# Performance work log

Measured on AMD Instinct MI355X. Metric: run time of the kernel, lower is better.

The kernel has to match this reference:

```python
import jax, jax.numpy as jnp
import numpy as np

B, C, H, W = 4, 64, 128, 128
DG = 16            # deformable groups
K = 9              # 3x3 kernel taps
MAX_RES = 10.0     # max_residue_magnitude


def conv3x3(x, w, b):
    y = jax.lax.conv_general_dilated(x, w, (1, 1), 'SAME',
                                     dimension_numbers=('NCHW', 'OIHW', 'NCHW'))
    return y + b[None, :, None, None]


def lrelu(x):
    return jnp.where(x >= 0, x, 0.1 * x)


def deform_conv(x, offset, mask, w, b):
    # x: [B,C,H,W]; offset: [B,2*DG*K,H,W] (dy,dx interleaved per tap); mask: [B,DG*K,H,W]
    Bx, Cx, Hx, Wx = x.shape
    Cg = Cx // DG
    off = offset.reshape(Bx, DG, K, 2, Hx, Wx)
    dy, dx = off[:, :, :, 0], off[:, :, :, 1]          # [B,DG,K,H,W]
    ky = (jnp.arange(K) // 3 - 1).astype(x.dtype)      # kernel tap row offsets (pad=1, dil=1)
    kx = (jnp.arange(K) % 3 - 1).astype(x.dtype)
    hh = jnp.arange(Hx, dtype=x.dtype)
    ww = jnp.arange(Wx, dtype=x.dtype)
    py = dy + ky[None, None, :, None, None] + hh[None, None, None, :, None]
    px = dx + kx[None, None, :, None, None] + ww[None, None, None, None, :]
    y0 = jnp.floor(py)
    x0 = jnp.floor(px)
    ly = py - y0
    lx = px - x0
    y0i = y0.astype(jnp.int32)
    x0i = x0.astype(jnp.int32)
    flat = x.reshape(Bx, DG, Cg, Hx * Wx)

    def gather(yi, xi):
        valid = (yi >= 0) & (yi < Hx) & (xi >= 0) & (xi < Wx)
        idx = jnp.clip(yi, 0, Hx - 1) * Wx + jnp.clip(xi, 0, Wx - 1)
        g = jnp.take_along_axis(flat, idx.reshape(Bx, DG, 1, K * Hx * Wx), axis=3)
        g = g.reshape(Bx, DG, Cg, K, Hx, Wx)
        return g * valid[:, :, None].astype(g.dtype)

    samp = (gather(y0i, x0i) * ((1 - ly) * (1 - lx))[:, :, None]
            + gather(y0i, x0i + 1) * ((1 - ly) * lx)[:, :, None]
            + gather(y0i + 1, x0i) * (ly * (1 - lx))[:, :, None]
            + gather(y0i + 1, x0i + 1) * (ly * lx)[:, :, None])   # [B,DG,Cg,K,H,W]
    samp = samp * mask.reshape(Bx, DG, 1, K, Hx, Wx)
    samp = samp.reshape(Bx, Cx, K, Hx, Wx)
    wk = w.reshape(w.shape[0], Cx, K)
    return jnp.einsum('bckhw,ock->bohw', samp, wk) + b[None, :, None, None]


def setup_inputs() -> dict:
    key = jax.random.key(0)
    ks = jax.random.split(key, 12)
    in_off = 2 * C + 2  # (1 + pa_frames//2)*C + pa_frames, pa_frames=2

    def n(k, shape, s=0.05):
        return jax.random.normal(k, shape, jnp.float32) * s

    return {
        'x': n(ks[0], (B, C, H, W), 1.0),
        'x_flow_warped': n(ks[1], (B, C, H, W), 1.0),
        'x_current': n(ks[2], (B, C, H, W), 1.0),
        'flow': n(ks[3], (B, 2, H, W), 1.0),
        'w0': n(ks[4], (C, in_off, 3, 3)), 'b0': jnp.zeros((C,), jnp.float32),
        'w1': n(ks[5], (C, C, 3, 3)), 'b1': jnp.zeros((C,), jnp.float32),
        'w2': n(ks[6], (C, C, 3, 3)), 'b2': jnp.zeros((C,), jnp.float32),
        'w3': n(ks[7], (3 * K * DG, C, 3, 3)), 'b3': jnp.zeros((3 * K * DG,), jnp.float32),
        'w_dcn': n(ks[8], (C, C, 3, 3)), 'b_dcn': jnp.zeros((C,), jnp.float32),
    }


def reference(x, x_flow_warped, x_current, flow,
              w0, b0, w1, b1, w2, b2, w3, b3, w_dcn, b_dcn):
    # conv_offset stack on [warped feats, current feats, flow]
    concat = jnp.concatenate([x_flow_warped, x_current, flow], axis=1)
    h = lrelu(conv3x3(concat, w0, b0))
    h = lrelu(conv3x3(h, w1, b1))
    h = lrelu(conv3x3(h, w2, b2))
    out = conv3x3(h, w3, b3)
    o1, o2, m = jnp.split(out, 3, axis=1)
    offset = MAX_RES * jnp.tanh(jnp.concatenate([o1, o2], axis=1))   # [B,2*DG*K,H,W]
    # pa_frames == 2: add flipped flow (dy,dx) to every tap's offset pair
    offset = offset + jnp.tile(flow[:, ::-1], (1, offset.shape[1] // 2, 1, 1))
    mask = jax.nn.sigmoid(m)
    return deform_conv(x, offset, mask, w_dcn, b_dcn)
```

## Files before the change

kernel.cpp:

```cpp
#include <hip/hip_runtime.h>
#include <hip/hip_bf16.h>
#include <cmath>

#define HH 128
#define WW 128
#define HWSZ (HH*WW)
#define BB 4
#define PH 130

typedef __attribute__((ext_vector_type(8))) short short8;
typedef __attribute__((ext_vector_type(4))) short sh4;
typedef _Float16 half8 __attribute__((ext_vector_type(8)));
typedef __attribute__((ext_vector_type(16))) float f32x16;

__device__ __forceinline__ ushort f16_rn(float f) {
    _Float16 h = (_Float16)f;
    return __builtin_bit_cast(ushort, h);
}
__device__ __forceinline__ float f16_f(ushort u) {
    return (float)__builtin_bit_cast(_Float16, u);
}
__device__ __forceinline__ float fast_tanh(float x) {
    const float e = __builtin_amdgcn_exp2f(x * 2.885390081777927f);
    return 1.f - 2.f * __builtin_amdgcn_rcpf(e + 1.f);
}
__device__ __forceinline__ float fast_sig(float x) {
    return __builtin_amdgcn_rcpf(1.f + __builtin_amdgcn_exp2f(-x * 1.4426950408889634f));
}

__global__ __launch_bounds__(256) void prep_wcm(const float* __restrict__ w,
                                                ushort* __restrict__ wOut,
                                                int ICREAL, int ICPAD) {
    const int ICSTEPS = ICPAD >> 4;
    int idx = blockIdx.x * 256 + threadIdx.x;
    if (idx >= 9 * ICSTEPS * 64 * 16) return;
    int j = idx & 7, lhi = (idx >> 3) & 1, oc = (idx >> 4) & 63, tk = idx >> 10;
    int tap = tk / ICSTEPS, ks = tk - tap * ICSTEPS;
    int ic = ks * 16 + lhi * 8 + j;
    float v = (ic < ICREAL) ? w[(size_t)oc * ICREAL * 9 + ic * 9 + tap] : 0.f;
    wOut[idx] = f16_rn(v);
}

__global__ __launch_bounds__(256) void prep_w3cm(const float* __restrict__ w,
                                                 ushort* __restrict__ wOut) {
    int idx = blockIdx.x * 256 + threadIdx.x;
    if (idx >= 36 * 512 * 16) return;
    int j = idx & 7, lhi = (idx >> 3) & 1, oc = (idx >> 4) & 511, tk = idx >> 13;
    int tap = tk >> 2, ks = tk & 3;
    int ic = ks * 16 + lhi * 8 + j;
    float v = (oc < 432) ? w[(size_t)oc * 576 + ic * 9 + tap] : 0.f;
    wOut[idx] = f16_rn(v);
}

__global__ __launch_bounds__(256) void prep_wdf_k(const float* __restrict__ w,
                                                  ushort* __restrict__ whiF) {
    int idx = blockIdx.x * 256 + threadIdx.x;
    if (idx >= 64 * 576) return;
    int oc = idx / 576, rem = idx - oc * 576;
    int k9 = rem / 64, c = rem & 63;
    float v = w[(size_t)oc * 576 + c * 9 + k9];
    const int hv = c >> 5, r = c & 31;
    const int ks = r >> 4, lhi = (r >> 3) & 1, j = r & 7;
    const size_t dst = (size_t)((k9 * 2 + hv) * 2 + ks) * 1024 + oc * 16 + lhi * 8 + j;
    whiF[dst] = f16_rn(v);
}

__global__ __launch_bounds__(256) void zero_border(ushort* __restrict__ buf, int C) {
    int idx = blockIdx.x * 256 + threadIdx.x;
    if (idx >= BB * 4 * PH * C) return;
    int c = idx % C;
    int r = idx / C;
    int pos = r % PH;
    int zone = (r / PH) & 3;
    int b = r / (PH * 4);
    int y, x;
    if (zone == 0)      { y = 0;      x = pos; }
    else if (zone == 1) { y = PH - 1; x = pos; }
    else if (zone == 2) { y = pos;    x = 0; }
    else                { y = pos;    x = PH - 1; }
    buf[(((size_t)b * PH + y) * PH + x) * C + c] = 0;
}

__global__ __launch_bounds__(256) void cvt_cm(const float* __restrict__ xfw,
                                              const float* __restrict__ xcur,
                                              const float* __restrict__ flow,
                                              ushort* __restrict__ out) {
    __shared__ ushort T[32][36];
    const int tid = threadIdx.x;
    const int b = blockIdx.x >> 7, y = blockIdx.x & 127;

    for (int c0 = 0; c0 < 144; c0 += 32) {
        for (int x0 = 0; x0 < 128; x0 += 32) {
            #pragma unroll
            for (int i = 0; i < 4; ++i) {
                const int cl = i * 8 + (tid >> 5);
                const int c = c0 + cl;
                const int x = x0 + (tid & 31);
                float v = 0.f;
                if (c < 64)       v = xfw [((size_t)b * 64 + c)       * HWSZ + y * WW + x];
                else if (c < 128) v = xcur[((size_t)b * 64 + c - 64)  * HWSZ + y * WW + x];
                else if (c < 130) v = flow[((size_t)b * 2  + c - 128) * HWSZ + y * WW + x];
                T[cl][tid & 31] = f16_rn(v);
            }
            __syncthreads();
            #pragma unroll
            for (int i = 0; i < 4; ++i) {
                const int xl = i * 8 + (tid >> 5);
                const int c = c0 + (tid & 31);
                if (c < 144)
                    out[(((size_t)b * PH + y + 1) * PH + x0 + xl + 1) * 144 + c] = T[tid & 31][xl];
            }
            __syncthreads();
        }
    }
}

__global__ __launch_bounds__(256) void pack_x_k(const float* __restrict__ x,
                                                sh4* __restrict__ xP) {
    int idx = blockIdx.x * 256 + threadIdx.x;
    if (idx >= BB * 16 * HWSZ) return;
    int b = idx / (16 * HWSZ);
    int rem = idx - b * 16 * HWSZ;
    int dg = rem / HWSZ, pix = rem - dg * HWSZ;
    const float* src = x + ((size_t)b * 64 + dg * 4) * HWSZ + pix;
    sh4 v;
    v[0] = (short)f16_rn(src[0]);
    v[1] = (short)f16_rn(src[HWSZ]);
    v[2] = (short)f16_rn(src[2 * HWSZ]);
    v[3] = (short)f16_rn(src[3 * HWSZ]);
    xP[idx] = v;
}

template<int ICPAD, int ICSTEPS>
__global__ __launch_bounds__(512, 4) void conv_cm(
    const ushort* __restrict__ actIn, const ushort* __restrict__ wT,
    const float* __restrict__ bias, ushort* __restrict__ actOut)
{
    constexpr int SYI = PH * ICPAD;
    const int tid = threadIdx.x;
    const int id  = blockIdx.x;
    const int orig = (id & 7) * 64 + (id >> 3);
    const int b = orig >> 7, y = orig & 127;

    const int wave = tid >> 6, lane = tid & 63;
    const int wm = wave >> 2, wn = wave & 3;
    const int l31 = lane & 31, lhi = lane >> 5;

    f32x16 acc = {};

    const ushort* arow = actIn + ((size_t)b * PH + y) * SYI
                       + (wn * 32 + l31) * ICPAD + lhi * 8;
    const ushort* wb = wT + (wm * 32 + l31) * 16 + lhi * 8;

    #pragma unroll
    for (int tap = 0; tap < 9; ++tap) {
        const int ky = tap / 3, kx = tap % 3;
        #pragma unroll
        for (int ks = 0; ks < ICSTEPS; ++ks) {
            const half8 af = __builtin_bit_cast(half8,
                *(const short8*)&arow[ky * SYI + kx * ICPAD + ks * 16]);
            const half8 wf = __builtin_bit_cast(half8,
                *(const short8*)&wb[(size_t)(tap * ICSTEPS + ks) * 1024]);
            acc = __builtin_amdgcn_mfma_f32_32x32x16_f16(af, wf, acc, 0, 0, 0);
        }
    }

    const int oc = wm * 32 + l31;
    const float bi = bias[oc];
    ushort* ob = actOut + (((size_t)b * PH + y + 1) * PH + 1) * 64 + oc;
    #pragma unroll
    for (int r = 0; r < 16; ++r) {
        const int px = wn * 32 + (r & 3) + 8 * (r >> 2) + 4 * lhi;
        float v = acc[r] + bi;
        v = v >= 0.f ? v : 0.1f * v;
        ob[(size_t)px * 64] = f16_rn(v);
    }
}

__global__ __launch_bounds__(512, 2) void conv_lds(
    const ushort* __restrict__ actIn, const ushort* __restrict__ wT,
    const float* __restrict__ bias, ushort* __restrict__ actOut)
{
    __shared__ ushort aS[3 * 130 * 64];

    const int tid = threadIdx.x;
    const int id  = blockIdx.x;
    const int orig = (id & 7) * 64 + (id >> 3);
    const int b = orig >> 7, y = orig & 127;

    const int wave = tid >> 6, lane = tid & 63;
    const int wm = wave >> 2, wn = wave & 3;
    const int l31 = lane & 31, lhi = lane >> 5;

    for (int i = tid; i < 3 * 130 * 8; i += 512) {
        const int seg = i & 7;
        const int px  = (i >> 3) % 130;
        const int row = (i >> 3) / 130;
        const ushort* src = actIn + (((size_t)b * PH + y + row) * PH + px) * 64 + seg * 8;
        const int d16 = (row * 130 + px) * 8 + (seg ^ (px & 7));
        *(short8*)&aS[d16 * 8] = *(const short8*)src;
    }
    __syncthreads();

    f32x16 acc = {};
    const ushort* wb = wT + (wm * 32 + l31) * 16 + lhi * 8;

    #pragma unroll
    for (int tap = 0; tap < 9; ++tap) {
        const int ky = tap / 3, kx = tap % 3;
        #pragma unroll
        for (int ks = 0; ks < 4; ++ks) {
            const int lpx = wn * 32 + l31 + kx;
            const int idx16 = (ky * 130 + lpx) * 8 + ((ks * 2 + lhi) ^ (lpx & 7));
            const half8 af = __builtin_bit_cast(half8,
                *(const short8*)&aS[idx16 * 8]);
            const half8 wf = __builtin_bit_cast(half8,
                *(const short8*)&wb[(size_t)(tap * 4 + ks) * 1024]);
            acc = __builtin_amdgcn_mfma_f32_32x32x16_f16(af, wf, acc, 0, 0, 0);
        }
    }

    const int oc = wm * 32 + l31;
    const float bi = bias[oc];
    ushort* ob = actOut + (((size_t)b * PH + y + 1) * PH + 1) * 64 + oc;
    #pragma unroll
    for (int r = 0; r < 16; ++r) {
        const int px = wn * 32 + (r & 3) + 8 * (r >> 2) + 4 * lhi;
        float v = acc[r] + bi;
        v = v >= 0.f ? v : 0.1f * v;
        ob[(size_t)px * 64] = f16_rn(v);
    }
}

__global__ __launch_bounds__(512, 4) void conv3_cm(
    const ushort* __restrict__ actIn, const ushort* __restrict__ wT3,
    const float* __restrict__ bias, uint* __restrict__ offP,
    ushort* __restrict__ mskP, const float* __restrict__ flow)
{
    __shared__ ushort aS[3 * 66 * 64];

    const int tid = threadIdx.x;
    const int id  = blockIdx.x;
    const int orig = (id & 7) * 128 + (id >> 3);
    const int xhalf = orig & 1;
    const int rid = orig >> 1;
    const int b = rid >> 7, y = rid & 127;
    const int xb = xhalf * 64;

    const int wave = tid >> 6, lane = tid & 63;
    const int l31 = lane & 31, lhi = lane >> 5;
    const int o0 = wave * 64;

    for (int i = tid; i < 3 * 66 * 8; i += 512) {
        const int seg = i & 7;
        const int px  = (i >> 3) % 66;
        const int row = (i >> 3) / 66;
        const ushort* src = actIn + (((size_t)b * PH + y + row) * PH + xb + px) * 64 + seg * 8;
        const int d16 = (row * 66 + px) * 8 + (seg ^ (px & 7));
        *(short8*)&aS[d16 * 8] = *(const short8*)src;
    }
    __syncthreads();

    f32x16 acc[2][2] = {};
    const ushort* wb = wT3 + (o0 + l31) * 16 + lhi * 8;

    #pragma unroll
    for (int tap = 0; tap < 9; ++tap) {
        const int ky = tap / 3, kx = tap % 3;
        #pragma unroll
        for (int ks = 0; ks < 4; ++ks) {
            const half8 af0 = __builtin_bit_cast(half8,
                *(const short8*)&wb[(size_t)(tap * 4 + ks) * 8192]);
            const half8 af1 = __builtin_bit_cast(half8,
                *(const short8*)&wb[(size_t)(tap * 4 + ks) * 8192 + 512]);
            #pragma unroll
            for (int pg = 0; pg < 2; ++pg) {
                const int lpx = pg * 32 + l31 + kx;
                const int idx16 = (ky * 66 + lpx) * 8 + ((ks * 2 + lhi) ^ (lpx & 7));
                const half8 bf = __builtin_bit_cast(half8,
                    *(const short8*)&aS[idx16 * 8]);
                acc[0][pg] = __builtin_amdgcn_mfma_f32_32x32x16_f16(af0, bf, acc[0][pg], 0, 0, 0);
                acc[1][pg] = __builtin_amdgcn_mfma_f32_32x32x16_f16(af1, bf, acc[1][pg], 0, 0, 0);
            }
        }
    }

    uint*   offb = offP + (size_t)b * 144 * HWSZ;
    ushort* mskb = mskP + (size_t)b * 144 * HWSZ;
    #pragma unroll
    for (int pg = 0; pg < 2; ++pg) {
        const int px = xb + pg * 32 + l31;
        const size_t pixb = (size_t)y * WW + px;
        const float fl0 = flow[((size_t)b * 2)     * HWSZ + pixb];
        const float fl1 = flow[((size_t)b * 2 + 1) * HWSZ + pixb];
        #pragma unroll
        for (int mg = 0; mg < 2; ++mg) {
            #pragma unroll
            for (int t = 0; t < 8; ++t) {
                const int r0 = 2 * t;
                const int oc = o0 + mg * 32 + (r0 & 3) + 8 * (r0 >> 2) + 4 * lhi;
                const float vy = acc[mg][pg][r0]     + bias[oc < 432 ? oc : 0];
                const float vx = acc[mg][pg][r0 + 1] + bias[oc < 431 ? oc + 1 : 0];
                if (oc < 288) {
                    const float ry = 10.f * fast_tanh(vy) + fl1;
                    const float rx = 10.f * fast_tanh(vx) + fl0;
                    offb[(size_t)(oc >> 1) * HWSZ + pixb] =
                        (uint)f16_rn(ry) | ((uint)f16_rn(rx) << 16);
                } else if (oc < 432) {
                    mskb[(size_t)(oc - 288) * HWSZ + pixb] = f16_rn(fast_sig(vy));
                    mskb[(size_t)(oc - 287) * HWSZ + pixb] = f16_rn(fast_sig(vx));
                }
            }
        }
    }
}

__global__ __launch_bounds__(512, 4) void deform_v11(
    const sh4* __restrict__ xP, const uint* __restrict__ offP,
    const ushort* __restrict__ mskP, const ushort* __restrict__ wdfh,
    const float* __restrict__ bias, float* __restrict__ outp)
{
    __shared__ float red[2][2][64][33];

    const int tid = threadIdx.x;
    const int id  = blockIdx.x;
    const int orig = (id & 7) * 128 + (id >> 3);
    const int x0 = (orig & 1) * 64;
    const int rl = orig >> 1;
    const int y = rl & 127, b = rl >> 7;

    const int wave = tid >> 6, lane = tid & 63;
    const int l31 = lane & 31, lhi = lane >> 5;
    const int pxh = wave >> 2;
    const int w4  = wave & 3;
    const int k9h = w4 >> 1;
    const int hv  = w4 & 1;

    const int xp  = x0 + pxh * 32 + l31;
    const int pix = y * WW + xp;
    const uint*   offb = offP + (size_t)b * 144 * HWSZ;
    const ushort* mskb = mskP + (size_t)b * 144 * HWSZ;
    const float fy = (float)y, fx = (float)xp;

    f32x16 acc[2] = {};

    const int k9lo = k9h ? 5 : 0;
    const int k9hi = k9h ? 9 : 5;
    for (int k9 = k9lo; k9 < k9hi; ++k9) {
        const float kyf = (float)(k9 / 3 - 1);
        const float kxf = (float)(k9 % 3 - 1);
        #pragma unroll
        for (int ks = 0; ks < 2; ++ks) {
            short8 bfs;
            #pragma unroll
            for (int d2 = 0; d2 < 2; ++d2) {
                const int dg = hv * 8 + ks * 4 + lhi * 2 + d2;
                const int m  = dg * 9 + k9;
                const uint u = offb[(size_t)m * HWSZ + pix];
                const float dy = f16_f((ushort)(u & 0xffffu));
                const float dx = f16_f((ushort)(u >> 16));
                const float mk = f16_f(mskb[(size_t)m * HWSZ + pix]);
                const float py = dy + kyf + fy;
                const float px = dx + kxf + fx;
                const float y0f = floorf(py), x0f = floorf(px);
                const float ly = py - y0f, lx = px - x0f;
                const int yi = (int)y0f, xi = (int)x0f;
                const float w00 = (1.f - ly) * (1.f - lx), w01 = (1.f - ly) * lx;
                const float w10 = ly * (1.f - lx),         w11 = ly * lx;
                const bool vy0 = (unsigned)yi < (unsigned)HH, vy1 = (unsigned)(yi + 1) < (unsigned)HH;
                const bool vx0 = (unsigned)xi < (unsigned)WW, vx1 = (unsigned)(xi + 1) < (unsigned)WW;
                const float f00 = (vy0 && vx0) ? w00 * mk : 0.f;
                const float f01 = (vy0 && vx1) ? w01 * mk : 0.f;
                const float f10 = (vy1 && vx0) ? w10 * mk : 0.f;
                const float f11 = (vy1 && vx1) ? w11 * mk : 0.f;
                const int cy0 = min(max(yi, 0), HH - 1), cy1 = min(max(yi + 1, 0), HH - 1);
                const int cx0 = min(max(xi, 0), WW - 1), cx1 = min(max(xi + 1, 0), WW - 1);
                const sh4* xg = xP + (size_t)(b * 16 + dg) * HWSZ;
                const sh4 c00 = xg[cy0 * WW + cx0], c01 = xg[cy0 * WW + cx1];
                const sh4 c10 = xg[cy1 * WW + cx0], c11 = xg[cy1 * WW + cx1];
                #pragma unroll
                for (int n = 0; n < 4; ++n) {
                    const float s = f00 * f16_f((ushort)c00[n]) + f01 * f16_f((ushort)c01[n])
                                  + f10 * f16_f((ushort)c10[n]) + f11 * f16_f((ushort)c11[n]);
                    bfs[d2 * 4 + n] = (short)f16_rn(s);
                }
            }
            const half8 bf = __builtin_bit_cast(half8, bfs);
            const size_t abase = (size_t)((k9 * 2 + hv) * 2 + ks) * 1024 + l31 * 16 + lhi * 8;
            #pragma unroll
            for (int mg = 0; mg < 2; ++mg) {
                const half8 ah = __builtin_bit_cast(half8, *(const short8*)&wdfh[abase + mg * 512]);
                acc[mg] = __builtin_amdgcn_mfma_f32_32x32x16_f16(ah, bf, acc[mg], 0, 0, 0);
            }
        }
    }

    if (w4 >= 2) {
        #pragma unroll
        for (int mg = 0; mg < 2; ++mg)
            #pragma unroll
            for (int r = 0; r < 16; ++r)
                red[pxh][w4 - 2][lane][mg * 16 + r] = acc[mg][r];
    }
    __syncthreads();
    if (w4 < 2) {
        #pragma unroll
        for (int mg = 0; mg < 2; ++mg)
            #pragma unroll
            for (int r = 0; r < 16; ++r)
                acc[mg][r] += red[pxh][w4][lane][mg * 16 + r];
    }
    __syncthreads();
    if (w4 == 1) {
        #pragma unroll
        for (int mg = 0; mg < 2; ++mg)
            #pragma unroll
            for (int r = 0; r < 16; ++r)
                red[pxh][0][lane][mg * 16 + r] = acc[mg][r];
    }
    __syncthreads();
    if (w4 == 0) {
        #pragma unroll
        for (int mg = 0; mg < 2; ++mg)
            #pragma unroll
            for (int r = 0; r < 16; ++r) {
                const int oc = mg * 32 + (r & 3) + 8 * (r >> 2) + 4 * lhi;
                const float v = acc[mg][r] + red[pxh][0][lane][mg * 16 + r] + bias[oc];
                outp[(((size_t)b * 64 + oc) * HH + y) * WW + xp] = v;
            }
    }
}

extern "C" void kernel_launch(void* const* d_in, const int* in_sizes, int n_in,
                              void* d_out, int out_size, void* d_ws, size_t ws_size,
                              hipStream_t stream) {
    const float* x    = (const float*)d_in[0];
    const float* xfw  = (const float*)d_in[1];
    const float* xcur = (const float*)d_in[2];
    const float* flow = (const float*)d_in[3];
    const float* w0   = (const float*)d_in[4];
    const float* b0   = (const float*)d_in[5];
    const float* w1   = (const float*)d_in[6];
    const float* b1   = (const float*)d_in[7];
    const float* w2   = (const float*)d_in[8];
    const float* b2   = (const float*)d_in[9];
    const float* w3   = (const float*)d_in[10];
    const float* b3   = (const float*)d_in[11];
    const float* wdcn = (const float*)d_in[12];
    const float* bdcn = (const float*)d_in[13];
    float* out = (float*)d_out;

    char* p = (char*)d_ws;
    uint*   offP    = (uint*)p;                         p += (size_t)BB * 144 * HWSZ * 4;
    ushort* mskP    = (ushort*)p;                       p += (size_t)BB * 144 * HWSZ * 2;
    ushort* h0A     = (ushort*)p;                       p += (size_t)BB * PH * PH * 64 * 2;
    ushort* h1A     = (ushort*)p;                       p += (size_t)BB * PH * PH * 64 * 2;
    ushort* concatA = (ushort*)p;                       p += (size_t)BB * PH * PH * 144 * 2;
    sh4*    xPh     = (sh4*)p;                          p += (size_t)BB * 16 * HWSZ * 8;
    ushort* wdh = (ushort*)p;                           p += 64 * 576 * 2;
    ushort* w0T = (ushort*)p;                           p += 9 * 9 * 64 * 16 * 2;
    ushort* w1T = (ushort*)p;                           p += 9 * 4 * 64 * 16 * 2;
    ushort* w2T = (ushort*)p;                           p += 9 * 4 * 64 * 16 * 2;
    ushort* w3T = (ushort*)p;                           p += 36 * 512 * 16 * 2;
    ushort* h2A = h0A;

    zero_border<<<dim3((BB * 4 * PH * 144 + 255) / 256), dim3(256), 0, stream>>>(concatA, 144);
    zero_border<<<dim3((BB * 4 * PH * 64 + 255) / 256),  dim3(256), 0, stream>>>(h0A, 64);
    zero_border<<<dim3((BB * 4 * PH * 64 + 255) / 256),  dim3(256), 0, stream>>>(h1A, 64);

    prep_wcm<<<dim3((9 * 9 * 64 * 16 + 255) / 256), dim3(256), 0, stream>>>(w0, w0T, 130, 144);
    prep_wcm<<<dim3((9 * 4 * 64 * 16 + 255) / 256), dim3(256), 0, stream>>>(w1, w1T, 64, 64);
    prep_wcm<<<dim3((9 * 4 * 64 * 16 + 255) / 256), dim3(256), 0, stream>>>(w2, w2T, 64, 64);
    prep_w3cm<<<dim3((36 * 512 * 16 + 255) / 256), dim3(256), 0, stream>>>(w3, w3T);
    prep_wdf_k<<<dim3((64 * 576 + 255) / 256), dim3(256), 0, stream>>>(wdcn, wdh);
    cvt_cm<<<dim3(BB * HH), dim3(256), 0, stream>>>(xfw, xcur, flow, concatA);
    pack_x_k<<<dim3((BB * 16 * HWSZ + 255) / 256), dim3(256), 0, stream>>>(x, xPh);

    conv_cm<144, 9><<<dim3(BB * HH), dim3(512), 0, stream>>>(concatA, w0T, b0, h0A);
    conv_lds<<<dim3(BB * HH), dim3(512), 0, stream>>>(h0A, w1T, b1, h1A);
    conv_lds<<<dim3(BB * HH), dim3(512), 0, stream>>>(h1A, w2T, b2, h2A);
    conv3_cm<<<dim3(BB * HH * 2), dim3(512), 0, stream>>>(h2A, w3T, b3, offP, mskP, flow);

    deform_v11<<<dim3(1024), dim3(512), 0, stream>>>(xPh, offP, mskP, wdh, bdcn, out);
}
```

Measured before the change: 223.6 us.

## Stage first conv input rows in LDS and split each row into half-width blocks

The first offset-network conv now copies its 3-row by 66-pixel input halo (144 channels) into shared memory, in a channel-segment-major layout, before running the MFMA loop. It no longer reads the activations straight from global memory for every tap. Each block now covers half an image row with 256 threads, so the grid doubles. This removes repeated global/L2 loads of overlapping tap windows, at the cost of a barrier and about 57KB of LDS per block, which limits how many blocks fit on a CU.

```diff
diff --git a/kernel.cpp b/kernel.cpp
--- a/kernel.cpp
+++ b/kernel.cpp
@@ -131,36 +131,48 @@
     xP[idx] = v;
 }
 
-template<int ICPAD, int ICSTEPS>
-__global__ __launch_bounds__(512, 4) void conv_cm(
+__global__ __launch_bounds__(256, 2) void conv0_lds(
     const ushort* __restrict__ actIn, const ushort* __restrict__ wT,
     const float* __restrict__ bias, ushort* __restrict__ actOut)
 {
-    constexpr int SYI = PH * ICPAD;
+    __shared__ ushort aS[18 * 3 * 66 * 8];
+
     const int tid = threadIdx.x;
     const int id  = blockIdx.x;
-    const int orig = (id & 7) * 64 + (id >> 3);
-    const int b = orig >> 7, y = orig & 127;
+    const int orig = (id & 7) * 128 + (id >> 3);
+    const int xhalf = orig & 1;
+    const int rid = orig >> 1;
+    const int b = rid >> 7, y = rid & 127;
+    const int xb = xhalf * 64;
 
     const int wave = tid >> 6, lane = tid & 63;
-    const int wm = wave >> 2, wn = wave & 3;
+    const int wm = wave >> 1, wn = wave & 1;
     const int l31 = lane & 31, lhi = lane >> 5;
 
+    for (int i = tid; i < 18 * 3 * 66; i += 256) {
+        const int seg = i % 18;
+        const int rp  = i / 18;
+        const int px  = rp % 66;
+        const int row = rp / 66;
+        const ushort* src = actIn + (((size_t)b * PH + y + row) * PH + xb + px) * 144 + seg * 8;
+        const int g = (seg * 3 + row) * 66 + px;
+        *(short8*)&aS[g * 8] = *(const short8*)src;
+    }
+    __syncthreads();
+
     f32x16 acc = {};
-
-    const ushort* arow = actIn + ((size_t)b * PH + y) * SYI
-                       + (wn * 32 + l31) * ICPAD + lhi * 8;
     const ushort* wb = wT + (wm * 32 + l31) * 16 + lhi * 8;
 
     #pragma unroll
     for (int tap = 0; tap < 9; ++tap) {
         const int ky = tap / 3, kx = tap % 3;
         #pragma unroll
-        for (int ks = 0; ks < ICSTEPS; ++ks) {
+        for (int ks = 0; ks < 9; ++ks) {
+            const int g = ((ks * 2 + lhi) * 3 + ky) * 66 + (wn * 32 + l31 + kx);
             const half8 af = __builtin_bit_cast(half8,
-                *(const short8*)&arow[ky * SYI + kx * ICPAD + ks * 16]);
+                *(const short8*)&aS[g * 8]);
             const half8 wf = __builtin_bit_cast(half8,
-                *(const short8*)&wb[(size_t)(tap * ICSTEPS + ks) * 1024]);
+                *(const short8*)&wb[(size_t)(tap * 9 + ks) * 1024]);
             acc = __builtin_amdgcn_mfma_f32_32x32x16_f16(af, wf, acc, 0, 0, 0);
         }
     }
@@ -170,7 +182,7 @@
     ushort* ob = actOut + (((size_t)b * PH + y + 1) * PH + 1) * 64 + oc;
     #pragma unroll
     for (int r = 0; r < 16; ++r) {
-        const int px = wn * 32 + (r & 3) + 8 * (r >> 2) + 4 * lhi;
+        const int px = xb + wn * 32 + (r & 3) + 8 * (r >> 2) + 4 * lhi;
         float v = acc[r] + bi;
         v = v >= 0.f ? v : 0.1f * v;
         ob[(size_t)px * 64] = f16_rn(v);
@@ -476,7 +488,7 @@
     cvt_cm<<<dim3(BB * HH), dim3(256), 0, stream>>>(xfw, xcur, flow, concatA);
     pack_x_k<<<dim3((BB * 16 * HWSZ + 255) / 256), dim3(256), 0, stream>>>(x, xPh);
 
-    conv_cm<144, 9><<<dim3(BB * HH), dim3(512), 0, stream>>>(concatA, w0T, b0, h0A);
+    conv0_lds<<<dim3(BB * HH * 2), dim3(256), 0, stream>>>(concatA, w0T, b0, h0A);
     conv_lds<<<dim3(BB * HH), dim3(512), 0, stream>>>(h0A, w1T, b1, h1A);
     conv_lds<<<dim3(BB * HH), dim3(512), 0, stream>>>(h1A, w2T, b2, h2A);
     conv3_cm<<<dim3(BB * HH * 2), dim3(512), 0, stream>>>(h2A, w3T, b3, offP, mskP, flow);
```

Result: faster. 210.5 us (median of 2 runs) (-5.8%).
